# Kernel tuning notes

Hardware: AMD Instinct MI355X
Metric: run time of the kernel (lower is better)

Reference implementation:

```python
import jax, jax.numpy as jnp
import numpy as np

B, C, T, E = 8, 64, 128, 256
TYPE_NUM, NF = 40, 128
KS = (5, 4, 3)
NEG = -1e10


def setup_inputs() -> dict:
    key = jax.random.key(0)
    ks = jax.random.split(key, 10)
    s = 0.02
    return {
        "query": jax.random.normal(ks[0], (C, E), jnp.float32),
        "context": jax.random.normal(ks[1], (B, T, E), jnp.float32),
        "mask": jax.random.randint(ks[2], (B, T), 0, 2, jnp.int32),
        "W_hidden": jax.random.normal(ks[3], (4 * E, 4 * E), jnp.float32) * s,
        "b_hidden": jnp.zeros((4 * E,), jnp.float32),
        "W_v": jax.random.normal(ks[4], (1, 4 * E), jnp.float32) * s,
        "b_v": jnp.zeros((1,), jnp.float32),
        "W_lin": jax.random.normal(ks[5], (E, 4 * E), jnp.float32) * s,
        "b_lin": jnp.zeros((E,), jnp.float32),
        "conv_w0": jax.random.normal(ks[6], (NF, E, KS[0]), jnp.float32) * s,
        "conv_b0": jnp.zeros((NF,), jnp.float32),
        "conv_w1": jax.random.normal(ks[7], (NF, E, KS[1]), jnp.float32) * s,
        "conv_b1": jnp.zeros((NF,), jnp.float32),
        "conv_w2": jax.random.normal(ks[8], (NF, E, KS[2]), jnp.float32) * s,
        "conv_b2": jnp.zeros((NF,), jnp.float32),
        "W_cnn": jax.random.normal(ks[9], (TYPE_NUM, NF * 3), jnp.float32) * s,
        "b_cnn": jnp.zeros((TYPE_NUM,), jnp.float32),
    }


def _pair_feat(a, b):
    # [.., e] x2 -> [.., 4e]: [a, b, |a-b|, a*b]
    return jnp.concatenate([a, b, jnp.abs(a - b), a * b], axis=-1)


def _conv1d(x, w, b):
    # x: [b, e, c], w: [f, e, k] (torch Conv1d layout) -> [b, f, c-k+1]
    y = jax.lax.conv_general_dilated(
        x, w, window_strides=(1,), padding="VALID",
        dimension_numbers=("NCH", "OIH", "NCH"))
    return y + b[None, :, None]


def reference(query, context, mask, W_hidden, b_hidden, W_v, b_v,
              W_lin, b_lin, conv_w0, conv_b0, conv_w1, conv_b1,
              conv_w2, conv_b2, W_cnn, b_cnn):
    b, t, e = context.shape
    c = query.shape[0]
    q_ = jnp.broadcast_to(query[None, :, None, :], (b, c, t, e))
    ctx_ = jnp.broadcast_to(context[:, None, :, :], (b, c, t, e))
    feat = _pair_feat(q_, ctx_)                                 # [b,c,t,4e]
    h = jnp.tanh(feat @ W_hidden.T + b_hidden)                  # [b,c,t,4e]
    scores = (h @ W_v.T + b_v)[..., 0]                          # [b,c,t]
    scores = jnp.where((mask < 1)[:, None, :], NEG, scores)
    attn = jax.nn.softmax(scores, axis=-1)                      # [b,c,t]
    g = jnp.einsum("bct,bte->bce", attn, context)               # [b,c,e]
    q2 = jnp.broadcast_to(query[None], (b, c, e))
    h2 = jnp.tanh(_pair_feat(q2, g) @ W_hidden.T + b_hidden)    # [b,c,4e]
    x = h2 @ W_lin.T + b_lin                                    # [b,c,e]
    xT = jnp.transpose(x, (0, 2, 1))                            # [b,e,c]
    pooled = []
    for w, bb in ((conv_w0, conv_b0), (conv_w1, conv_b1), (conv_w2, conv_b2)):
        y = jax.nn.relu(_conv1d(xT, w, bb))                     # [b,f,c-k+1]
        pooled.append(jnp.max(y, axis=2))                       # [b,f]
    cnn = jnp.concatenate(pooled, axis=1)                       # [b,3f]
    return cnn @ W_cnn.T + b_cnn                                # [b,type_num]
```

## Files before the change

### kernel.cpp

```cpp
#include <hip/hip_runtime.h>
#include <math.h>


typedef __bf16 bf16x8 __attribute__((ext_vector_type(8)));
typedef float  f32x4  __attribute__((ext_vector_type(4)));

__device__ __forceinline__ float ftanh(float v) {
    float t = __expf(2.f * v);
    return 1.f - 2.f * __builtin_amdgcn_rcpf(t + 1.f);
}

__device__ __forceinline__ void gld_lds16(const __bf16* g, __bf16* l) {
    __builtin_amdgcn_global_load_lds(
        (const __attribute__((address_space(1))) void*)g,
        (__attribute__((address_space(3))) void*)l, 16, 0, 0);
}

__global__ __launch_bounds__(256) void gemm_tn_kernel(
    const float* __restrict__ A, int lda,
    const float* __restrict__ B, int ldb,
    const float* __restrict__ bias,
    float* __restrict__ C, int ldc, int K)
{
    __shared__ float As[16][68];
    __shared__ float Bs[16][68];
    const int tid = threadIdx.x;
    const int m0 = blockIdx.y * 64, n0 = blockIdx.x * 64;
    const int tm = tid >> 4, tn = tid & 15;
    const int lr = tid >> 2;
    const int lc = (tid & 3) * 4;

    float acc[4][4];
#pragma unroll
    for (int i = 0; i < 4; ++i)
#pragma unroll
        for (int j = 0; j < 4; ++j) acc[i][j] = 0.f;

    for (int k0 = 0; k0 < K; k0 += 16) {
        float4 av = *reinterpret_cast<const float4*>(A + (size_t)(m0 + lr) * lda + k0 + lc);
        float4 bv = *reinterpret_cast<const float4*>(B + (size_t)(n0 + lr) * ldb + k0 + lc);
        As[lc + 0][lr] = av.x; As[lc + 1][lr] = av.y; As[lc + 2][lr] = av.z; As[lc + 3][lr] = av.w;
        Bs[lc + 0][lr] = bv.x; Bs[lc + 1][lr] = bv.y; Bs[lc + 2][lr] = bv.z; Bs[lc + 3][lr] = bv.w;
        __syncthreads();
#pragma unroll
        for (int kk = 0; kk < 16; ++kk) {
            float4 a = *reinterpret_cast<const float4*>(&As[kk][tm * 4]);
            float4 b = *reinterpret_cast<const float4*>(&Bs[kk][tn * 4]);
            float ar[4] = {a.x, a.y, a.z, a.w};
            float br[4] = {b.x, b.y, b.z, b.w};
#pragma unroll
            for (int i = 0; i < 4; ++i)
#pragma unroll
                for (int j = 0; j < 4; ++j) acc[i][j] += ar[i] * br[j];
        }
        __syncthreads();
    }

#pragma unroll
    for (int i = 0; i < 4; ++i) {
        int m = m0 + tm * 4 + i;
        float vals[4];
#pragma unroll
        for (int j = 0; j < 4; ++j) {
            int n = n0 + tn * 4 + j;
            vals[j] = acc[i][j] + (bias ? bias[n] : 0.f);
        }
        float4 o; o.x = vals[0]; o.y = vals[1]; o.z = vals[2]; o.w = vals[3];
        *reinterpret_cast<float4*>(C + (size_t)m * ldc + n0 + tn * 4) = o;
    }
}

__global__ void cvt_kernel(const float* __restrict__ Wh, const float* __restrict__ Wl,
                           const float* __restrict__ ctx,
                           const float* __restrict__ cw0, const float* __restrict__ cw1,
                           const float* __restrict__ cw2,
                           __bf16* __restrict__ Whbf, __bf16* __restrict__ Whbf_t,
                           __bf16* __restrict__ Wlbf, __bf16* __restrict__ ctxbf,
                           float* __restrict__ wt0, float* __restrict__ wt1,
                           float* __restrict__ wt2)
{
    int idx = blockIdx.x * 256 + threadIdx.x;
    if (idx < 1048576) { Whbf[idx] = (__bf16)Wh[idx]; return; }
    if (idx < 1114112) {
        int di = idx - 1048576;
        int nc = di >> 14, rem = di & 16383;
        int kc = rem >> 11, row = (rem >> 3) & 255, kgp = rem & 7;
        int kg = kgp ^ (row & 7);
        const float* s = Wh + (size_t)(nc * 256 + row) * 1024 + 512 + kc * 64 + kg * 8;
        bf16x8 u;
#pragma unroll
        for (int i = 0; i < 8; ++i) u[i] = (__bf16)s[i];
        *reinterpret_cast<bf16x8*>(Whbf_t + (size_t)di * 8) = u;
        return;
    }
    if (idx < 1376256) { int j = idx - 1114112; Wlbf[j] = (__bf16)Wl[j]; return; }
    if (idx < 1409024) {
        int di = idx - 1376256;
        const float* s = ctx + (size_t)di * 8;
        bf16x8 u;
#pragma unroll
        for (int i = 0; i < 8; ++i) u[i] = (__bf16)s[i];
        *reinterpret_cast<bf16x8*>(ctxbf + (size_t)di * 8) = u;
        return;
    }
    if (idx < 1572864) {
        int j = idx - 1409024; int f = j & 127, rest = j >> 7;
        int i = rest % 5, e = rest / 5;
        wt0[j] = cw0[(size_t)(f * 256 + e) * 5 + i]; return;
    }
    if (idx < 1703936) {
        int j = idx - 1572864; int f = j & 127, rest = j >> 7;
        int i = rest & 3, e = rest >> 2;
        wt1[j] = cw1[(size_t)(f * 256 + e) * 4 + i]; return;
    }
    {
        int j = idx - 1703936; int f = j & 127, rest = j >> 7;
        int i = rest % 3, e = rest / 3;
        wt2[j] = cw2[(size_t)(f * 256 + e) * 3 + i];
    }
}

__global__ __launch_bounds__(256, 2) void attn_kernel(
    const float* __restrict__ q,
    const float* __restrict__ ctx,
    const int*   __restrict__ mask,
    const __bf16* __restrict__ Whbf_t,
    const float* __restrict__ Wv,
    const float* __restrict__ bv,
    const float* __restrict__ Apre,
    const float* __restrict__ Bpre,
    float* __restrict__ g)
{
    __shared__ __bf16 Us[128 * 64];
    __shared__ __bf16 Ws[256 * 64];
    __shared__ float qc[256];
    __shared__ float sc[128];
    __shared__ float red;

    const int tid = threadIdx.x;
    const int b = blockIdx.x >> 6, c = blockIdx.x & 63;
    const int wave = tid >> 6, lane = tid & 63;
    const int w0 = wave >> 1, w1 = wave & 1;
    const int m0 = w0 * 64;
    const int l15 = lane & 15, quad = lane >> 4;
    const int swz = l15 & 7;
    const int kg = tid & 7;

    qc[tid] = q[c * 256 + tid];
    if (tid < 128) sc[tid] = 0.f;
    __syncthreads();

    for (int nc = 0; nc < 4; ++nc) {
        f32x4 acc[4][8];
#pragma unroll
        for (int mi = 0; mi < 4; ++mi)
#pragma unroll
            for (int ni = 0; ni < 8; ++ni) acc[mi][ni] = (f32x4){0.f, 0.f, 0.f, 0.f};

        for (int kc = 0; kc < 8; ++kc) {
            const bool isabs = (kc < 4);
            const int e0 = (kc & 3) * 64;
            const int eb = e0 + kg * 8;
            float qv8[8];
#pragma unroll
            for (int i = 0; i < 8; ++i) qv8[i] = qc[eb + i];
            bf16x8 u[4];
#pragma unroll
            for (int it = 0; it < 4; ++it) {
                int t = (tid + it * 256) >> 3;
                const float* cp = ctx + (size_t)(b * 128 + t) * 256 + eb;
                float4 c0 = *reinterpret_cast<const float4*>(cp);
                float4 c1 = *reinterpret_cast<const float4*>(cp + 4);
                float cv[8] = {c0.x, c0.y, c0.z, c0.w, c1.x, c1.y, c1.z, c1.w};
#pragma unroll
                for (int i = 0; i < 8; ++i) {
                    float x = isabs ? fabsf(qv8[i] - cv[i]) : qv8[i] * cv[i];
                    u[it][i] = (__bf16)x;
                }
            }
            __syncthreads();
            const __bf16* wtile = Whbf_t + (size_t)(nc * 8 + kc) * 16384;
#pragma unroll
            for (int it = 0; it < 8; ++it) {
                int gidx = wave * 512 + it * 64;
                gld_lds16(wtile + (size_t)(gidx + lane) * 8, &Ws[gidx * 8]);
            }
#pragma unroll
            for (int it = 0; it < 4; ++it) {
                int t = (tid + it * 256) >> 3;
                *reinterpret_cast<bf16x8*>(&Us[t * 64 + (kg ^ (t & 7)) * 8]) = u[it];
            }
            __syncthreads();
#pragma unroll
            for (int ks = 0; ks < 2; ++ks) {
                const int c8 = (((ks * 4 + quad) ^ swz)) * 8;
                bf16x8 a[4], bf[8];
#pragma unroll
                for (int mi = 0; mi < 4; ++mi)
                    a[mi] = *reinterpret_cast<const bf16x8*>(
                        &Us[(m0 + mi * 16 + l15) * 64 + c8]);
#pragma unroll
                for (int ni = 0; ni < 8; ++ni)
                    bf[ni] = *reinterpret_cast<const bf16x8*>(
                        &Ws[(w1 * 128 + ni * 16 + l15) * 64 + c8]);
#pragma unroll
                for (int mi = 0; mi < 4; ++mi)
#pragma unroll
                    for (int ni = 0; ni < 8; ++ni)
                        acc[mi][ni] = __builtin_amdgcn_mfma_f32_16x16x32_bf16(
                            a[mi], bf[ni], acc[mi][ni], 0, 0, 0);
            }
        }

        const int jcol = nc * 256 + w1 * 128 + l15;
        float av[8], wv[8];
#pragma unroll
        for (int ni = 0; ni < 8; ++ni) {
            av[ni] = Apre[c * 1024 + jcol + ni * 16];
            wv[ni] = Wv[jcol + ni * 16];
        }
#pragma unroll
        for (int mi = 0; mi < 4; ++mi) {
            const int tbase = m0 + mi * 16 + quad * 4;
            float p[4];
#pragma unroll
            for (int r = 0; r < 4; ++r) {
                const float* bp = Bpre + (size_t)(b * 128 + tbase + r) * 1024 + jcol;
                float s = 0.f;
#pragma unroll
                for (int ni = 0; ni < 8; ++ni)
                    s += ftanh(acc[mi][ni][r] + av[ni] + bp[ni * 16]) * wv[ni];
                p[r] = s;
            }
#pragma unroll
            for (int off = 1; off < 16; off <<= 1)
#pragma unroll
                for (int r = 0; r < 4; ++r) p[r] += __shfl_xor(p[r], off, 16);
            if (l15 == 0) {
#pragma unroll
                for (int r = 0; r < 4; ++r) atomicAdd(&sc[tbase + r], p[r]);
            }
        }
        __syncthreads();
    }

    if (tid < 128) {
        float s = sc[tid] + bv[0];
        if (mask[b * 128 + tid] < 1) s = -1e10f;
        sc[tid] = s;
    }
    __syncthreads();
    if (tid < 64) {
        float m = fmaxf(sc[tid], sc[tid + 64]);
        for (int off = 32; off; off >>= 1) m = fmaxf(m, __shfl_xor(m, off, 64));
        if (tid == 0) red = m;
    }
    __syncthreads();
    const float mx = red;
    if (tid < 128) sc[tid] = __expf(sc[tid] - mx);
    __syncthreads();
    if (tid < 64) {
        float s = sc[tid] + sc[tid + 64];
        for (int off = 32; off; off >>= 1) s += __shfl_xor(s, off, 64);
        if (tid == 0) red = s;
    }
    __syncthreads();
    const float inv = 1.f / red;

    float gv = 0.f;
    for (int t = 0; t < 128; ++t) gv += sc[t] * ctx[(size_t)(b * 128 + t) * 256 + tid];
    g[(size_t)blockIdx.x * 256 + tid] = gv * inv;
}

__global__ void feat2_kernel(const float* __restrict__ q, const float* __restrict__ g,
                             __bf16* __restrict__ feat2)
{
    int row = blockIdx.x, e = threadIdx.x;
    int c = row & 63;
    float qv = q[c * 256 + e], gv = g[row * 256 + e];
    __bf16* o = feat2 + (size_t)row * 768 + e;
    o[0]   = (__bf16)gv;
    o[256] = (__bf16)fabsf(qv - gv);
    o[512] = (__bf16)(qv * gv);
}

template <int ACT, int OUTBF, int BMODE>
__global__ __launch_bounds__(256) void mfma_gemm_kernel(
    const __bf16* __restrict__ A, int lda,
    const __bf16* __restrict__ B, int ldb,
    const float* __restrict__ bias, void* __restrict__ Cout,
    int K, int ldc)
{
    __shared__ __bf16 As[64 * 72];
    __shared__ __bf16 Bs[64 * 72];
    const int tid = threadIdx.x;
    const int wave = tid >> 6, lane = tid & 63;
    const int w0 = wave >> 1, w1 = wave & 1;
    const int l15 = lane & 15, quad = lane >> 4;
    const int m0 = blockIdx.y * 64, n0 = blockIdx.x * 64;

    f32x4 acc[2][2];
#pragma unroll
    for (int mi = 0; mi < 2; ++mi)
#pragma unroll
        for (int ni = 0; ni < 2; ++ni) acc[mi][ni] = (f32x4){0.f, 0.f, 0.f, 0.f};

    for (int k0 = 0; k0 < K; k0 += 64) {
        __syncthreads();
#pragma unroll
        for (int it = 0; it < 2; ++it) {
            int idx = tid + it * 256;
            int row = idx >> 3, kgi = idx & 7;
            int4 va = *reinterpret_cast<const int4*>(A + (size_t)(m0 + row) * lda + k0 + kgi * 8);
            *reinterpret_cast<int4*>(&As[row * 72 + kgi * 8]) = va;
            int4 vb = *reinterpret_cast<const int4*>(B + (size_t)(n0 + row) * ldb + k0 + kgi * 8);
            *reinterpret_cast<int4*>(&Bs[row * 72 + kgi * 8]) = vb;
        }
        __syncthreads();
#pragma unroll
        for (int ks = 0; ks < 2; ++ks) {
            bf16x8 a[2], bb[2];
#pragma unroll
            for (int mi = 0; mi < 2; ++mi)
                a[mi] = *reinterpret_cast<const bf16x8*>(
                    &As[(w0 * 32 + mi * 16 + l15) * 72 + ks * 32 + quad * 8]);
#pragma unroll
            for (int ni = 0; ni < 2; ++ni)
                bb[ni] = *reinterpret_cast<const bf16x8*>(
                    &Bs[(w1 * 32 + ni * 16 + l15) * 72 + ks * 32 + quad * 8]);
#pragma unroll
            for (int mi = 0; mi < 2; ++mi)
#pragma unroll
                for (int ni = 0; ni < 2; ++ni)
                    acc[mi][ni] = __builtin_amdgcn_mfma_f32_16x16x32_bf16(
                        a[mi], bb[ni], acc[mi][ni], 0, 0, 0);
        }
    }

#pragma unroll
    for (int mi = 0; mi < 2; ++mi)
#pragma unroll
        for (int ni = 0; ni < 2; ++ni) {
            int col = n0 + w1 * 32 + ni * 16 + l15;
#pragma unroll
            for (int r = 0; r < 4; ++r) {
                int row = m0 + w0 * 32 + mi * 16 + quad * 4 + r;
                float bsv = (BMODE == 0) ? bias[col]
                          : (BMODE == 1) ? bias[(row & 63) * 1024 + col] : 0.f;
                float v = acc[mi][ni][r] + bsv;
                if (ACT) v = ftanh(v);
                if (OUTBF) ((__bf16*)Cout)[(size_t)row * ldc + col] = (__bf16)v;
                else       ((float*)Cout)[(size_t)row * ldc + col] = v;
            }
        }
}

template <int KW>
__device__ __forceinline__ void conv_body(
    const float* __restrict__ x, const float* __restrict__ wt,
    float* __restrict__ part, int b, int chunk, int bi, float* xs)
{
    const int tid = threadIdx.x;
    const int f = tid & 127, esub = tid >> 7;
    const int e0 = chunk * 64;

#pragma unroll
    for (int it = 0; it < 16; ++it) {
        int idx = tid + it * 256;
        int e = idx & 63, p = idx >> 6;
        xs[e * 72 + p] = x[(size_t)(b * 64 + p) * 256 + e0 + e];
    }
    __syncthreads();

    float acc[64];
#pragma unroll
    for (int p = 0; p < 64; ++p) acc[p] = 0.f;

    for (int ei = 0; ei < 32; ++ei) {
        const int eL = esub * 32 + ei;
        float wreg[KW];
#pragma unroll
        for (int i = 0; i < KW; ++i)
            wreg[i] = wt[(size_t)((e0 + eL) * KW + i) * 128 + f];
        float xv[68];
#pragma unroll
        for (int k4 = 0; k4 < 17; ++k4) {
            float4 v = *reinterpret_cast<const float4*>(&xs[eL * 72 + k4 * 4]);
            xv[k4 * 4 + 0] = v.x; xv[k4 * 4 + 1] = v.y;
            xv[k4 * 4 + 2] = v.z; xv[k4 * 4 + 3] = v.w;
        }
#pragma unroll
        for (int i = 0; i < KW; ++i)
#pragma unroll
            for (int p = 0; p < 64; ++p)
                acc[p] = fmaf(wreg[i], xv[p + i], acc[p]);
    }

    float* op = part + ((size_t)(bi * 2 + esub)) * 8192 + f;
#pragma unroll
    for (int p = 0; p < 64; ++p) op[p * 128] = acc[p];
}

__global__ __launch_bounds__(256) void conv_partial_kernel(
    const float* __restrict__ x,
    const float* __restrict__ wt0, const float* __restrict__ wt1,
    const float* __restrict__ wt2, float* __restrict__ part)
{
    __shared__ float xs[64 * 72];
    const int bi = blockIdx.x;
    const int kw = bi >> 5, b = (bi >> 2) & 7, chunk = bi & 3;
    if (kw == 0)      conv_body<5>(x, wt0, part, b, chunk, bi, xs);
    else if (kw == 1) conv_body<4>(x, wt1, part, b, chunk, bi, xs);
    else              conv_body<3>(x, wt2, part, b, chunk, bi, xs);
}

__global__ __launch_bounds__(128) void reduce_pool_kernel(
    const float* __restrict__ part,
    const float* __restrict__ b0, const float* __restrict__ b1,
    const float* __restrict__ b2, float* __restrict__ cnn)
{
    const int bi = blockIdx.x;
    const int kw = bi >> 3, b = bi & 7;
    const int f = threadIdx.x;
    const int KW = 5 - kw, P = 64 - KW + 1;
    const float bias = (kw == 0 ? b0 : kw == 1 ? b1 : b2)[f];
    float mx = 0.f;
    for (int p = 0; p < P; ++p) {
        float s = 0.f;
#pragma unroll
        for (int c4 = 0; c4 < 4; ++c4)
#pragma unroll
            for (int es = 0; es < 2; ++es)
                s += part[((size_t)((kw * 32 + b * 4 + c4) * 2 + es)) * 8192 + p * 128 + f];
        s += bias;
        mx = fmaxf(mx, s);
    }
    cnn[b * 384 + kw * 128 + f] = mx;
}

__global__ void final_kernel(const float* __restrict__ cnn, const float* __restrict__ Wc,
                             const float* __restrict__ bc, float* __restrict__ out)
{
    int o = threadIdx.x;
    if (o >= 320) return;
    int b = o / 40, t = o - b * 40;
    float s = bc[t];
    for (int i = 0; i < 384; ++i) s += cnn[b * 384 + i] * Wc[t * 384 + i];
    out[o] = s;
}

extern "C" void kernel_launch(void* const* d_in, const int* in_sizes, int n_in,
                              void* d_out, int out_size, void* d_ws, size_t ws_size,
                              hipStream_t stream)
{
    (void)in_sizes; (void)n_in; (void)out_size; (void)ws_size;
    const float* q    = (const float*)d_in[0];
    const float* ctx  = (const float*)d_in[1];
    const int*   mask = (const int*)d_in[2];
    const float* Wh   = (const float*)d_in[3];
    const float* bh   = (const float*)d_in[4];
    const float* Wv   = (const float*)d_in[5];
    const float* bv   = (const float*)d_in[6];
    const float* Wl   = (const float*)d_in[7];
    const float* bl   = (const float*)d_in[8];
    const float* cw0  = (const float*)d_in[9];
    const float* cb0  = (const float*)d_in[10];
    const float* cw1  = (const float*)d_in[11];
    const float* cb1  = (const float*)d_in[12];
    const float* cw2  = (const float*)d_in[13];
    const float* cb2  = (const float*)d_in[14];
    const float* Wc   = (const float*)d_in[15];
    const float* bc   = (const float*)d_in[16];

    float* ws   = (float*)d_ws;
    float* Apre = ws;
    float* g    = Apre + 65536;
    float* x    = g + 131072;
    float* cnn  = x + 131072;
    float* part = cnn + 3072;
    float* wt0  = part + 1572864;
    float* wt1  = wt0 + 163840;
    float* wt2  = wt1 + 131072;
    __bf16* bfb    = (__bf16*)(wt2 + 98304);
    __bf16* Whbf   = bfb;
    __bf16* Wlbf   = bfb + 1048576;
    __bf16* feat2b = bfb + 1310720;
    __bf16* h2b    = bfb + 1703936;
    __bf16* Whbf_t = (__bf16*)part;
    __bf16* ctxbf  = Whbf_t + 524288;
    float*  Bpre   = (float*)(ctxbf + 262144);

    dim3 blk(256);
    cvt_kernel<<<7040, blk, 0, stream>>>(Wh, Wl, ctx, cw0, cw1, cw2,
                                         Whbf, Whbf_t, Wlbf, ctxbf, wt0, wt1, wt2);
    gemm_tn_kernel<<<dim3(16, 1), blk, 0, stream>>>(q, 256, Wh, 1024, bh, Apre, 1024, 256);
    mfma_gemm_kernel<0, 0, 2><<<dim3(16, 16), blk, 0, stream>>>(
        ctxbf, 256, Whbf + 256, 1024, nullptr, Bpre, 256, 1024);
    attn_kernel<<<512, blk, 0, stream>>>(q, ctx, mask, Whbf_t, Wv, bv, Apre, Bpre, g);
    feat2_kernel<<<512, blk, 0, stream>>>(q, g, feat2b);
    mfma_gemm_kernel<1, 1, 1><<<dim3(16, 8), blk, 0, stream>>>(
        feat2b, 768, Whbf + 256, 1024, Apre, h2b, 768, 1024);
    mfma_gemm_kernel<0, 0, 0><<<dim3(4, 8), blk, 0, stream>>>(
        h2b, 1024, Wlbf, 1024, bl, x, 1024, 256);
    conv_partial_kernel<<<96, blk, 0, stream>>>(x, wt0, wt1, wt2, part);
    reduce_pool_kernel<<<24, 128, 0, stream>>>(part, cb0, cb1, cb2, cnn);
    final_kernel<<<1, 320, 0, stream>>>(cnn, Wc, bc, (float*)d_out);
}
```

Before: 319.5 us.

## Process two queries per attention block and split hidden dim across blocks

The attention scoring kernel now handles a pair of query rows per 512-thread block, sharing each Whbf_t weight tile load across both queries, and splits the 1024 hidden columns into two halves across blocks. Partial scores are accumulated into a global buffer with atomics, and a separate tail kernel does masking, softmax and the context weighted sum. This halves weight-tile traffic per query and raises parallelism, at the cost of an extra kernel launch, global atomics, and zero-initialising the score buffer in the conversion kernel.

```diff
diff --git a/kernel.cpp b/kernel.cpp
--- a/kernel.cpp
+++ b/kernel.cpp
@@ -77,7 +77,7 @@
                            __bf16* __restrict__ Whbf, __bf16* __restrict__ Whbf_t,
                            __bf16* __restrict__ Wlbf, __bf16* __restrict__ ctxbf,
                            float* __restrict__ wt0, float* __restrict__ wt1,
-                           float* __restrict__ wt2)
+                           float* __restrict__ wt2, float* __restrict__ gsc)
 {
     int idx = blockIdx.x * 256 + threadIdx.x;
     if (idx < 1048576) { Whbf[idx] = (__bf16)Wh[idx]; return; }
@@ -113,44 +113,44 @@
         int i = rest & 3, e = rest >> 2;
         wt1[j] = cw1[(size_t)(f * 256 + e) * 4 + i]; return;
     }
-    {
+    if (idx < 1802240) {
         int j = idx - 1703936; int f = j & 127, rest = j >> 7;
         int i = rest % 3, e = rest / 3;
-        wt2[j] = cw2[(size_t)(f * 256 + e) * 3 + i];
-    }
-}
-
-__global__ __launch_bounds__(256, 2) void attn_kernel(
+        wt2[j] = cw2[(size_t)(f * 256 + e) * 3 + i]; return;
+    }
+    gsc[idx - 1802240] = 0.f;
+}
+
+__global__ __launch_bounds__(512, 4) void attn_mfma_kernel(
     const float* __restrict__ q,
     const float* __restrict__ ctx,
-    const int*   __restrict__ mask,
     const __bf16* __restrict__ Whbf_t,
     const float* __restrict__ Wv,
-    const float* __restrict__ bv,
     const float* __restrict__ Apre,
     const float* __restrict__ Bpre,
-    float* __restrict__ g)
-{
-    __shared__ __bf16 Us[128 * 64];
+    float* __restrict__ gsc)
+{
+    __shared__ __bf16 Us[256 * 64];
     __shared__ __bf16 Ws[256 * 64];
-    __shared__ float qc[256];
-    __shared__ float sc[128];
-    __shared__ float red;
+    __shared__ float qc[512];
+    __shared__ float sc[256];
 
     const int tid = threadIdx.x;
-    const int b = blockIdx.x >> 6, c = blockIdx.x & 63;
+    const int cpair = blockIdx.x >> 1, nh = blockIdx.x & 1;
+    const int b = cpair >> 5, c0 = (cpair & 31) * 2;
     const int wave = tid >> 6, lane = tid & 63;
-    const int w0 = wave >> 1, w1 = wave & 1;
+    const int w1 = wave & 1, w0 = wave >> 1;
     const int m0 = w0 * 64;
     const int l15 = lane & 15, quad = lane >> 4;
     const int swz = l15 & 7;
     const int kg = tid & 7;
 
-    qc[tid] = q[c * 256 + tid];
-    if (tid < 128) sc[tid] = 0.f;
+    qc[tid] = q[(size_t)(c0 + (tid >> 8)) * 256 + (tid & 255)];
+    if (tid < 256) sc[tid] = 0.f;
     __syncthreads();
 
-    for (int nc = 0; nc < 4; ++nc) {
+    for (int nci = 0; nci < 2; ++nci) {
+        const int nc = nh * 2 + nci;
         f32x4 acc[4][8];
 #pragma unroll
         for (int mi = 0; mi < 4; ++mi)
@@ -161,71 +161,74 @@
             const bool isabs = (kc < 4);
             const int e0 = (kc & 3) * 64;
             const int eb = e0 + kg * 8;
-            float qv8[8];
-#pragma unroll
-            for (int i = 0; i < 8; ++i) qv8[i] = qc[eb + i];
-            bf16x8 u[4];
-#pragma unroll
-            for (int it = 0; it < 4; ++it) {
-                int t = (tid + it * 256) >> 3;
-                const float* cp = ctx + (size_t)(b * 128 + t) * 256 + eb;
-                float4 c0 = *reinterpret_cast<const float4*>(cp);
-                float4 c1 = *reinterpret_cast<const float4*>(cp + 4);
-                float cv[8] = {c0.x, c0.y, c0.z, c0.w, c1.x, c1.y, c1.z, c1.w};
+            float qA[8], qB[8];
+#pragma unroll
+            for (int i = 0; i < 8; ++i) { qA[i] = qc[eb + i]; qB[i] = qc[256 + eb + i]; }
+            bf16x8 u0[2], u1[2];
+#pragma unroll
+            for (int it = 0; it < 2; ++it) {
+                const int trow = it * 64 + (tid >> 3);
+                const float* cp = ctx + (size_t)(b * 128 + trow) * 256 + eb;
+                float4 cl0 = *reinterpret_cast<const float4*>(cp);
+                float4 cl1 = *reinterpret_cast<const float4*>(cp + 4);
+                float cv[8] = {cl0.x, cl0.y, cl0.z, cl0.w, cl1.x, cl1.y, cl1.z, cl1.w};
 #pragma unroll
                 for (int i = 0; i < 8; ++i) {
-                    float x = isabs ? fabsf(qv8[i] - cv[i]) : qv8[i] * cv[i];
-                    u[it][i] = (__bf16)x;
+                    u0[it][i] = (__bf16)(isabs ? fabsf(qA[i] - cv[i]) : qA[i] * cv[i]);
+                    u1[it][i] = (__bf16)(isabs ? fabsf(qB[i] - cv[i]) : qB[i] * cv[i]);
                 }
             }
             __syncthreads();
             const __bf16* wtile = Whbf_t + (size_t)(nc * 8 + kc) * 16384;
 #pragma unroll
-            for (int it = 0; it < 8; ++it) {
-                int gidx = wave * 512 + it * 64;
+            for (int it = 0; it < 4; ++it) {
+                int gidx = wave * 256 + it * 64;
                 gld_lds16(wtile + (size_t)(gidx + lane) * 8, &Ws[gidx * 8]);
             }
 #pragma unroll
-            for (int it = 0; it < 4; ++it) {
-                int t = (tid + it * 256) >> 3;
-                *reinterpret_cast<bf16x8*>(&Us[t * 64 + (kg ^ (t & 7)) * 8]) = u[it];
+            for (int it = 0; it < 2; ++it) {
+                const int trow = it * 64 + (tid >> 3);
+                const int off = (kg ^ (trow & 7)) * 8;
+                *reinterpret_cast<bf16x8*>(&Us[trow * 64 + off]) = u0[it];
+                *reinterpret_cast<bf16x8*>(&Us[(trow + 128) * 64 + off]) = u1[it];
             }
             __syncthreads();
 #pragma unroll
             for (int ks = 0; ks < 2; ++ks) {
                 const int c8 = (((ks * 4 + quad) ^ swz)) * 8;
-                bf16x8 a[4], bf[8];
+                bf16x8 a[4], bfr[8];
 #pragma unroll
                 for (int mi = 0; mi < 4; ++mi)
                     a[mi] = *reinterpret_cast<const bf16x8*>(
                         &Us[(m0 + mi * 16 + l15) * 64 + c8]);
 #pragma unroll
                 for (int ni = 0; ni < 8; ++ni)
-                    bf[ni] = *reinterpret_cast<const bf16x8*>(
+                    bfr[ni] = *reinterpret_cast<const bf16x8*>(
                         &Ws[(w1 * 128 + ni * 16 + l15) * 64 + c8]);
 #pragma unroll
                 for (int mi = 0; mi < 4; ++mi)
 #pragma unroll
                     for (int ni = 0; ni < 8; ++ni)
                         acc[mi][ni] = __builtin_amdgcn_mfma_f32_16x16x32_bf16(
-                            a[mi], bf[ni], acc[mi][ni], 0, 0, 0);
+                            a[mi], bfr[ni], acc[mi][ni], 0, 0, 0);
             }
         }
 
         const int jcol = nc * 256 + w1 * 128 + l15;
+        const int c = c0 + (w0 >> 1);
         float av[8], wv[8];
 #pragma unroll
         for (int ni = 0; ni < 8; ++ni) {
-            av[ni] = Apre[c * 1024 + jcol + ni * 16];
+            av[ni] = Apre[(size_t)c * 1024 + jcol + ni * 16];
             wv[ni] = Wv[jcol + ni * 16];
         }
 #pragma unroll
         for (int mi = 0; mi < 4; ++mi) {
-            const int tbase = m0 + mi * 16 + quad * 4;
+            const int tb = (w0 & 1) * 64 + mi * 16 + quad * 4;
             float p[4];
 #pragma unroll
             for (int r = 0; r < 4; ++r) {
-                const float* bp = Bpre + (size_t)(b * 128 + tbase + r) * 1024 + jcol;
+                const float* bp = Bpre + (size_t)(b * 128 + tb + r) * 1024 + jcol;
                 float s = 0.f;
 #pragma unroll
                 for (int ni = 0; ni < 8; ++ni)
@@ -238,14 +241,28 @@
                 for (int r = 0; r < 4; ++r) p[r] += __shfl_xor(p[r], off, 16);
             if (l15 == 0) {
 #pragma unroll
-                for (int r = 0; r < 4; ++r) atomicAdd(&sc[tbase + r], p[r]);
+                for (int r = 0; r < 4; ++r)
+                    atomicAdd(&sc[(w0 >> 1) * 128 + tb + r], p[r]);
             }
         }
         __syncthreads();
     }
 
+    if (tid < 256) atomicAdd(&gsc[(size_t)(b * 64 + c0) * 128 + tid], sc[tid]);
+}
+
+__global__ __launch_bounds__(256) void attn_tail_kernel(
+    const float* __restrict__ ctx, const int* __restrict__ mask,
+    const float* __restrict__ bv, const float* __restrict__ gsc,
+    float* __restrict__ g)
+{
+    __shared__ float sc[128];
+    __shared__ float red;
+    const int tid = threadIdx.x;
+    const int bc = blockIdx.x, b = bc >> 6;
+
     if (tid < 128) {
-        float s = sc[tid] + bv[0];
+        float s = gsc[(size_t)bc * 128 + tid] + bv[0];
         if (mask[b * 128 + tid] < 1) s = -1e10f;
         sc[tid] = s;
     }
@@ -269,7 +286,7 @@
 
     float gv = 0.f;
     for (int t = 0; t < 128; ++t) gv += sc[t] * ctx[(size_t)(b * 128 + t) * 256 + tid];
-    g[(size_t)blockIdx.x * 256 + tid] = gv * inv;
+    g[(size_t)bc * 256 + tid] = gv * inv;
 }
 
 __global__ void feat2_kernel(const float* __restrict__ q, const float* __restrict__ g,
@@ -486,17 +503,19 @@
     __bf16* Wlbf   = bfb + 1048576;
     __bf16* feat2b = bfb + 1310720;
     __bf16* h2b    = bfb + 1703936;
+    float*  gsc    = (float*)(bfb + 2228224);
     __bf16* Whbf_t = (__bf16*)part;
     __bf16* ctxbf  = Whbf_t + 524288;
     float*  Bpre   = (float*)(ctxbf + 262144);
 
     dim3 blk(256);
-    cvt_kernel<<<7040, blk, 0, stream>>>(Wh, Wl, ctx, cw0, cw1, cw2,
-                                         Whbf, Whbf_t, Wlbf, ctxbf, wt0, wt1, wt2);
+    cvt_kernel<<<7296, blk, 0, stream>>>(Wh, Wl, ctx, cw0, cw1, cw2,
+                                         Whbf, Whbf_t, Wlbf, ctxbf, wt0, wt1, wt2, gsc);
     gemm_tn_kernel<<<dim3(16, 1), blk, 0, stream>>>(q, 256, Wh, 1024, bh, Apre, 1024, 256);
     mfma_gemm_kernel<0, 0, 2><<<dim3(16, 16), blk, 0, stream>>>(
         ctxbf, 256, Whbf + 256, 1024, nullptr, Bpre, 256, 1024);
-    attn_kernel<<<512, blk, 0, stream>>>(q, ctx, mask, Whbf_t, Wv, bv, Apre, Bpre, g);
+    attn_mfma_kernel<<<512, dim3(512), 0, stream>>>(q, ctx, Whbf_t, Wv, Apre, Bpre, gsc);
+    attn_tail_kernel<<<512, blk, 0, stream>>>(ctx, mask, bv, gsc, g);
     feat2_kernel<<<512, blk, 0, stream>>>(q, g, feat2b);
     mfma_gemm_kernel<1, 1, 1><<<dim3(16, 8), blk, 0, stream>>>(
         feat2b, 768, Whbf + 256, 1024, Apre, h2b, 768, 1024);
```

Result: slower. 920.6 us (+188.2%).
